# Optimization experiments

Hardware: AMD Instinct MI355X
Metric: run time of the kernel (lower is better)

Reference implementation:

```python
import jax, jax.numpy as jnp
import numpy as np

N = 100000      # nodes
E = 1600000     # edges
F_IN = 64       # num_features
H = 64          # hidden_channels
NG = 64         # graphs in batch
ALPHA = 0.5


def _lin_init(key, fan_in, fan_out):
    kw, kb = jax.random.split(key)
    bound = 1.0 / np.sqrt(fan_in)
    w = jax.random.uniform(kw, (fan_in, fan_out), jnp.float32, -bound, bound)
    b = jax.random.uniform(kb, (fan_out,), jnp.float32, -bound, bound)
    return w, b


def setup_inputs() -> dict:
    key = jax.random.key(0)
    ks = jax.random.split(key, 12)
    x = jax.random.normal(ks[0], (N, F_IN), dtype=jnp.float32)
    edge_index = jax.random.randint(ks[1], (2, E), 0, N, dtype=jnp.int32)
    batch = jnp.sort(jax.random.randint(ks[2], (N,), 0, NG, dtype=jnp.int32))
    w1s, b1s = _lin_init(ks[3], F_IN, H)
    w1d, b1d = _lin_init(ks[4], F_IN, H)
    w2s, b2s = _lin_init(ks[5], H, H)
    w2d, b2d = _lin_init(ks[6], H, H)
    w3s, b3s = _lin_init(ks[7], H, H)
    w3d, b3d = _lin_init(ks[8], H, H)
    wl1, bl1 = _lin_init(ks[9], H, 5)
    wl2, bl2 = _lin_init(ks[10], 5, 1)
    return dict(x=x, edge_index=edge_index, batch=batch,
                w1s=w1s, b1s=b1s, w1d=w1d, b1d=b1d,
                w2s=w2s, b2s=b2s, w2d=w2d, b2d=b2d,
                w3s=w3s, b3s=b3s, w3d=w3d, b3d=b3d,
                wl1=wl1, bl1=bl1, wl2=wl2, bl2=bl2)


def _dir_gcn_conv(x, row, col, ws, bs, wd, bd):
    # directional norm: D_out^{-1/2} A D_in^{-1/2} (and same recipe for A^T)
    ones = jnp.ones((row.shape[0],), x.dtype)
    deg_out = jax.ops.segment_sum(ones, row, num_segments=N)  # row-sums of A
    deg_in = jax.ops.segment_sum(ones, col, num_segments=N)   # col-sums of A
    r_out = jnp.where(deg_out > 0, deg_out ** -0.5, 0.0)
    r_in = jnp.where(deg_in > 0, deg_in ** -0.5, 0.0)
    norm = r_out[row] * r_in[col]  # per-edge weight; identical for A and A^T norms
    msg = norm[:, None] * x[col]                       # [E, F]
    adj_x = jax.ops.segment_sum(msg, row, num_segments=N)
    msg_t = norm[:, None] * x[row]
    adj_t_x = jax.ops.segment_sum(msg_t, col, num_segments=N)
    return ALPHA * (adj_x @ ws + bs) + (1.0 - ALPHA) * (adj_t_x @ wd + bd)


def reference(x, edge_index, batch,
              w1s, b1s, w1d, b1d,
              w2s, b2s, w2d, b2d,
              w3s, b3s, w3d, b3d,
              wl1, bl1, wl2, bl2):
    row, col = edge_index[0], edge_index[1]
    h = jax.nn.relu(_dir_gcn_conv(x, row, col, w1s, b1s, w1d, b1d))
    h = jax.nn.relu(_dir_gcn_conv(h, row, col, w2s, b2s, w2d, b2d))
    h = jax.nn.relu(_dir_gcn_conv(h, row, col, w3s, b3s, w3d, b3d))
    g = jax.ops.segment_max(h, batch, num_segments=NG)  # global max pool [NG, H]
    g = jax.nn.relu(g @ wl1 + bl1)
    return g @ wl2 + bl2  # [NG, 1]
```

## Files before the change

### kernel.cpp

```cpp
#include <hip/hip_runtime.h>

#define N_NODES 100000
#define N_EDGES 1600000
#define EPAD    (N_EDGES + NB * BW + 512)
#define HDIM    64
#define NGRAPH  64
#define BW      256
#define NB      391
#define NBLK    256
#define CHUNK   ((N_EDGES + NBLK - 1) / NBLK)
#define MTILES  (N_NODES / 16)

typedef _Float16 h16;
typedef _Float16 h16x4 __attribute__((ext_vector_type(4)));
typedef _Float16 h16x8 __attribute__((ext_vector_type(8)));
typedef float    f32x4 __attribute__((ext_vector_type(4)));

__global__ __launch_bounds__(512) void bucket_count(const int* __restrict__ ei,
                                                    int* __restrict__ cntTabA,
                                                    int* __restrict__ cntTabT) {
    __shared__ int cA[NB], cT[NB];
    const int tid = threadIdx.x;
    for (int i = tid; i < NB; i += 512) { cA[i] = 0; cT[i] = 0; }
    __syncthreads();
    const int e0 = blockIdx.x * CHUNK, e1 = min(e0 + CHUNK, N_EDGES);
    for (int e = e0 + tid; e < e1; e += 512) {
        int r = ei[e];
        int c = ei[N_EDGES + e];
        atomicAdd(&cA[r >> 8], 1);
        atomicAdd(&cT[c >> 8], 1);
    }
    __syncthreads();
    for (int b = tid; b < NB; b += 512) {
        cntTabA[b * NBLK + blockIdx.x] = cA[b];
        cntTabT[b * NBLK + blockIdx.x] = cT[b];
    }
}

__global__ __launch_bounds__(256) void chunk_scan(int* __restrict__ cntTabA,
                                                  int* __restrict__ cntTabT,
                                                  int* __restrict__ tot) {
    __shared__ int s[256];
    const int b = blockIdx.x, d = blockIdx.y, tid = threadIdx.x;
    int* tab = d ? cntTabT : cntTabA;
    int v = tab[b * NBLK + tid];
    s[tid] = v;
    __syncthreads();
    for (int off = 1; off < 256; off <<= 1) {
        int t = (tid >= off) ? s[tid - off] : 0;
        __syncthreads();
        s[tid] += t;
        __syncthreads();
    }
    tab[b * NBLK + tid] = s[tid] - v;
    if (tid == 255) tot[d * 512 + b] = s[255];
}

__global__ __launch_bounds__(512) void start_scan(const int* __restrict__ tot,
                                                  int* __restrict__ bktStartA,
                                                  int* __restrict__ bktStartT) {
    __shared__ int s[512];
    const int tid = threadIdx.x;
    int v = (tid < NB) ? tot[tid] : 0;
    s[tid] = v;
    __syncthreads();
    for (int off = 1; off < 512; off <<= 1) {
        int t = (tid >= off) ? s[tid - off] : 0;
        __syncthreads();
        s[tid] += t;
        __syncthreads();
    }
    if (tid < NB) bktStartA[tid] = s[tid] - v;
    if (tid == 0) bktStartA[NB] = N_EDGES;
    __syncthreads();
    int v2 = (tid < NB) ? tot[512 + tid] : 0;
    s[tid] = v2;
    __syncthreads();
    for (int off = 1; off < 512; off <<= 1) {
        int t = (tid >= off) ? s[tid - off] : 0;
        __syncthreads();
        s[tid] += t;
        __syncthreads();
    }
    if (tid < NB) bktStartT[tid] = s[tid] - v2;
    if (tid == 0) bktStartT[NB] = N_EDGES;
}

__global__ __launch_bounds__(512) void bucketize_write(const int* __restrict__ ei,
                                                       const int* __restrict__ cntTabA,
                                                       const int* __restrict__ cntTabT,
                                                       const int* __restrict__ bktStartA,
                                                       const int* __restrict__ bktStartT,
                                                       int2* __restrict__ bktA,
                                                       int2* __restrict__ bktT) {
    __shared__ int bA[NB], bT[NB];
    const int tid = threadIdx.x;
    for (int i = tid; i < NB; i += 512) {
        bA[i] = bktStartA[i] + cntTabA[i * NBLK + blockIdx.x];
        bT[i] = bktStartT[i] + cntTabT[i * NBLK + blockIdx.x];
    }
    __syncthreads();
    const int e0 = blockIdx.x * CHUNK, e1 = min(e0 + CHUNK, N_EDGES);
    for (int e = e0 + tid; e < e1; e += 512) {
        int r = ei[e];
        int c = ei[N_EDGES + e];
        int pA = atomicAdd(&bA[r >> 8], 1);
        bktA[pA] = make_int2(r, c);
        int pT = atomicAdd(&bT[c >> 8], 1);
        bktT[pT] = make_int2(c, r);
    }
}

__global__ __launch_bounds__(256) void bucket_deg_ptr(
        const int* __restrict__ bktStartA, const int* __restrict__ bktStartT,
        const int2* __restrict__ bktA, const int2* __restrict__ bktT,
        int* __restrict__ deg_out, int* __restrict__ deg_in,
        float* __restrict__ r_out, float* __restrict__ r_in,
        int* __restrict__ rowptrP, int* __restrict__ colptrP) {
    __shared__ int c[BW];
    __shared__ int s[256];
    const int b = blockIdx.x, d = blockIdx.y, tid = threadIdx.x;
    const int* bs = d ? bktStartT : bktStartA;
    const int2* bkt = d ? bktT : bktA;
    int* deg = d ? deg_in : deg_out;
    float* rr = d ? r_in : r_out;
    int* ptr = d ? colptrP : rowptrP;
    const int node0 = b * BW;
    c[tid] = 0;
    __syncthreads();
    const int i0 = bs[b], i1 = bs[b + 1];
    for (int i = i0 + tid; i < i1; i += 256) atomicAdd(&c[bkt[i].x - node0], 1);
    __syncthreads();
    int n = node0 + tid, dg = c[tid];
    int pad = dg + (dg & 1);
    if (n < N_NODES) {
        deg[n] = dg;
        rr[n] = dg > 0 ? rsqrtf((float)dg) : 0.0f;
    } else pad = 0;
    s[tid] = pad;
    __syncthreads();
    for (int off = 1; off < 256; off <<= 1) {
        int t = (tid >= off) ? s[tid - off] : 0;
        __syncthreads();
        s[tid] += t;
        __syncthreads();
    }
    if (n < N_NODES) ptr[n] = i0 + b * BW + (s[tid] - pad);
}

__global__ __launch_bounds__(512) void bucket_scatter(
        const int* __restrict__ rowptrP, const int* __restrict__ colptrP,
        const float* __restrict__ r_out, const float* __restrict__ r_in,
        const int* __restrict__ bktStartA, const int* __restrict__ bktStartT,
        const int2* __restrict__ bktA, const int2* __restrict__ bktT,
        int2* __restrict__ recA, int2* __restrict__ recT) {
    __shared__ int cur[BW];
    __shared__ float rwt[BW];
    const int b = blockIdx.x, d = blockIdx.y, tid = threadIdx.x;
    const int* ptr = d ? colptrP : rowptrP;
    const float* rt = d ? r_in : r_out;
    const float* rs = d ? r_out : r_in;
    const int* bs = d ? bktStartT : bktStartA;
    const int2* bkt = d ? bktT : bktA;
    int2* rec = d ? recT : recA;
    const int node0 = b * BW;
    if (tid < BW) {
        int n = node0 + tid;
        cur[tid] = (n < N_NODES) ? ptr[n] : 0;
        rwt[tid] = (n < N_NODES) ? rt[n] : 0.0f;
    }
    __syncthreads();
    const int i0 = bs[b], i1 = bs[b + 1];
    for (int i = i0 + tid; i < i1; i += 512) {
        int2 e = bkt[i];
        float w = rwt[e.x - node0] * rs[e.y];
        int p = atomicAdd(&cur[e.x - node0], 1);
        rec[p] = make_int2(e.y << 7, __float_as_int(w));
    }
}

__global__ __launch_bounds__(256) void cast_kernel(const float4* __restrict__ x,
                                                   h16x4* __restrict__ xh,
                                                   unsigned* __restrict__ g) {
    if (blockIdx.x == 0) {
        for (int j = threadIdx.x; j < NGRAPH * HDIM; j += 256) g[j] = 0u;
    }
    int i = blockIdx.x * 256 + threadIdx.x;
    if (i < N_NODES * 16) {
        float4 v = x[i];
        h16x4 o;
        o.x = (h16)v.x; o.y = (h16)v.y; o.z = (h16)v.z; o.w = (h16)v.w;
        xh[i] = o;
    }
}

__global__ __launch_bounds__(256) void wprep_kernel(
        const float* __restrict__ w1s, const float* __restrict__ w1d,
        const float* __restrict__ w2s, const float* __restrict__ w2d,
        const float* __restrict__ w3s, const float* __restrict__ w3d,
        const float* __restrict__ b1s, const float* __restrict__ b1d,
        const float* __restrict__ b2s, const float* __restrict__ b2d,
        const float* __restrict__ b3s, const float* __restrict__ b3d,
        h16* __restrict__ WT, float* __restrict__ bc) {
    const int l = blockIdx.y;
    const float* ws = l == 0 ? w1s : l == 1 ? w2s : w3s;
    const float* wd = l == 0 ? w1d : l == 1 ? w2d : w3d;
    int e = blockIdx.x * 256 + threadIdx.x;
    if (e < 8192) {
        int f = e >> 7, k = e & 127;
        float v = (k < 64) ? ws[k * 64 + f] : wd[(k - 64) * 64 + f];
        WT[l * 8192 + f * 128 + k] = (h16)(0.5f * v);
    }
    if (blockIdx.x == 0 && threadIdx.x < 64) {
        const float* bs = l == 0 ? b1s : l == 1 ? b2s : b3s;
        const float* bd = l == 0 ? b1d : l == 1 ? b2d : b3d;
        bc[l * 64 + threadIdx.x] = 0.5f * (bs[threadIdx.x] + bd[threadIdx.x]);
    }
}

__device__ __forceinline__ void fma4h(float4& a, float w, h16x4 f) {
    a.x = fmaf(w, (float)f.x, a.x);
    a.y = fmaf(w, (float)f.y, a.y);
    a.z = fmaf(w, (float)f.z, a.z);
    a.w = fmaf(w, (float)f.w, a.w);
}

__device__ __forceinline__ float4 red_s(float4 v) {
    v.x += __shfl_xor(v.x, 16); v.y += __shfl_xor(v.y, 16);
    v.z += __shfl_xor(v.z, 16); v.w += __shfl_xor(v.w, 16);
    v.x += __shfl_xor(v.x, 32); v.y += __shfl_xor(v.y, 32);
    v.z += __shfl_xor(v.z, 32); v.w += __shfl_xor(v.w, 32);
    return v;
}

__device__ __forceinline__ h16x4 ld_h4(const char* __restrict__ p) {
    return *(const h16x4*)p;
}

__device__ __forceinline__ float4 agg_dir(const char* __restrict__ hb,
                                          const int2* __restrict__ rec,
                                          int start, int deg, int q, int s, int sh) {
    float4 a0 = {0.f,0.f,0.f,0.f}, a1 = {0.f,0.f,0.f,0.f};
    float4 a2 = {0.f,0.f,0.f,0.f}, a3 = {0.f,0.f,0.f,0.f};
    const int4* rec4 = (const int4*)(rec + start);
    const int qb = q * 8;
    const int t = 2 * s;
    int4 p0 = rec4[s];
    int4 p1 = rec4[4 + s];
    int4 p2 = rec4[8 + s];
    if (t < deg)      fma4h(a0, __int_as_float(p0.y), ld_h4(hb + (p0.x << sh) + qb));
    if (t + 1 < deg)  fma4h(a1, __int_as_float(p0.w), ld_h4(hb + (p0.z << sh) + qb));
    if (t + 8 < deg)  fma4h(a2, __int_as_float(p1.y), ld_h4(hb + (p1.x << sh) + qb));
    if (t + 9 < deg)  fma4h(a3, __int_as_float(p1.w), ld_h4(hb + (p1.z << sh) + qb));
    if (t + 16 < deg) fma4h(a0, __int_as_float(p2.y), ld_h4(hb + (p2.x << sh) + qb));
    if (t + 17 < deg) fma4h(a1, __int_as_float(p2.w), ld_h4(hb + (p2.z << sh) + qb));
    for (int k = 24; k < deg; k += 16) {
        int4 q0 = rec4[(k >> 1) + s];
        int4 q1 = rec4[(k >> 1) + 4 + s];
        if (k + t < deg)
            fma4h(a2, __int_as_float(q0.y), ld_h4(hb + (q0.x << sh) + qb));
        if (k + t + 1 < deg)
            fma4h(a3, __int_as_float(q0.w), ld_h4(hb + (q0.z << sh) + qb));
        if (k + t + 8 < deg)
            fma4h(a0, __int_as_float(q1.y), ld_h4(hb + (q1.x << sh) + qb));
        if (k + t + 9 < deg)
            fma4h(a1, __int_as_float(q1.w), ld_h4(hb + (q1.z << sh) + qb));
    }
    a0.x += a1.x; a0.y += a1.y; a0.z += a1.z; a0.w += a1.w;
    a2.x += a3.x; a2.y += a3.y; a2.z += a3.z; a2.w += a3.w;
    a0.x += a2.x; a0.y += a2.y; a0.z += a2.z; a0.w += a2.w;
    return red_s(a0);
}

__global__ __launch_bounds__(256) void agg_kernel(
        const char* __restrict__ h_in, char* __restrict__ acc_out, int sh,
        const int* __restrict__ rowptrP, const int* __restrict__ deg_out,
        const int2* __restrict__ recA,
        const int* __restrict__ colptrP, const int* __restrict__ deg_in,
        const int2* __restrict__ recT) {
    const int tid  = threadIdx.x;
    const int wid  = (blockIdx.x << 2) + (tid >> 6);
    const int lane = tid & 63;
    const int node = wid >> 1;
    const int dir  = wid & 1;
    const int q = lane & 15;
    const int s = lane >> 4;

    const int* ptr = dir ? colptrP : rowptrP;
    const int* deg = dir ? deg_in : deg_out;
    const int2* rec = dir ? recT : recA;

    float4 a = agg_dir(h_in, rec, ptr[node], deg[node], q, s, sh);
    if (s == 0) {
        h16x4 pk;
        pk.x = (h16)a.x; pk.y = (h16)a.y; pk.z = (h16)a.z; pk.w = (h16)a.w;
        *(h16x4*)(acc_out + (size_t)node * 256 + dir * 128 + q * 8) = pk;
    }
}

__global__ __launch_bounds__(256) void gemm_kernel(char* __restrict__ acc,
                                                   const h16* __restrict__ WT,
                                                   const float* __restrict__ bc,
                                                   const int* __restrict__ batch,
                                                   unsigned* __restrict__ g,
                                                   int do_pool) {
    const int lane = threadIdx.x & 63;
    const int wid = (blockIdx.x * 256 + threadIdx.x) >> 6;
    const int nW = gridDim.x * 4;
    const int m = lane & 15, t = lane >> 4;

    h16x8 bfrag[4][4];
    float bb[4];
#pragma unroll
    for (int nt = 0; nt < 4; nt++) {
        bb[nt] = bc[nt * 16 + m];
#pragma unroll
        for (int kk = 0; kk < 4; kk++)
            bfrag[nt][kk] = *(const h16x8*)(WT + (nt * 16 + m) * 128 + kk * 32 + t * 8);
    }

    for (int tile = wid; tile < MTILES; tile += nW) {
        char* arow = acc + (size_t)tile * 16 * 256;
        const int node0 = tile * 16;
        int b0 = 0, b15 = 0;
        if (do_pool) { b0 = batch[node0]; b15 = batch[node0 + 15]; }
        h16x8 afrag[4];
#pragma unroll
        for (int kk = 0; kk < 4; kk++)
            afrag[kk] = *(const h16x8*)(arow + m * 256 + kk * 64 + t * 16);
#pragma unroll
        for (int nt = 0; nt < 4; nt++) {
            f32x4 c = {0.f, 0.f, 0.f, 0.f};
#pragma unroll
            for (int kk = 0; kk < 4; kk++)
                c = __builtin_amdgcn_mfma_f32_16x16x32_f16(afrag[kk], bfrag[nt][kk], c, 0, 0, 0);
            float ov[4];
#pragma unroll
            for (int r = 0; r < 4; r++) {
                ov[r] = fmaxf(c[r] + bb[nt], 0.0f);
                *(h16*)(arow + (t * 4 + r) * 256 + (nt * 16 + m) * 2) = (h16)ov[r];
            }
            if (do_pool) {
                if (b0 == b15) {
                    float mx = fmaxf(fmaxf(ov[0], ov[1]), fmaxf(ov[2], ov[3]));
                    mx = fmaxf(mx, __shfl_xor(mx, 16));
                    mx = fmaxf(mx, __shfl_xor(mx, 32));
                    if (t == 0)
                        atomicMax(&g[b0 * HDIM + nt * 16 + m], __float_as_uint(mx));
                } else {
#pragma unroll
                    for (int r = 0; r < 4; r++)
                        atomicMax(&g[batch[node0 + t * 4 + r] * HDIM + nt * 16 + m],
                                  __float_as_uint(ov[r]));
                }
            }
        }
    }
}

__global__ __launch_bounds__(64) void mlp_kernel(const unsigned* __restrict__ g,
                                                 const float* __restrict__ wl1,
                                                 const float* __restrict__ bl1,
                                                 const float* __restrict__ wl2,
                                                 const float* __restrict__ bl2,
                                                 float* __restrict__ out) {
    int t = threadIdx.x;
    float gv[HDIM];
#pragma unroll
    for (int k = 0; k < HDIM; k++) gv[k] = __uint_as_float(g[t * HDIM + k]);
    float o = bl2[0];
#pragma unroll
    for (int j = 0; j < 5; j++) {
        float hj = bl1[j];
#pragma unroll
        for (int k = 0; k < HDIM; k++) hj += gv[k] * wl1[k * 5 + j];
        hj = fmaxf(hj, 0.0f);
        o += hj * wl2[j];
    }
    out[t] = o;
}

extern "C" void kernel_launch(void* const* d_in, const int* in_sizes, int n_in,
                              void* d_out, int out_size, void* d_ws, size_t ws_size,
                              hipStream_t stream) {
    const float* x   = (const float*)d_in[0];
    const int*   ei  = (const int*)d_in[1];
    const int*   bat = (const int*)d_in[2];
    const float* w1s = (const float*)d_in[3];
    const float* b1s = (const float*)d_in[4];
    const float* w1d = (const float*)d_in[5];
    const float* b1d = (const float*)d_in[6];
    const float* w2s = (const float*)d_in[7];
    const float* b2s = (const float*)d_in[8];
    const float* w2d = (const float*)d_in[9];
    const float* b2d = (const float*)d_in[10];
    const float* w3s = (const float*)d_in[11];
    const float* b3s = (const float*)d_in[12];
    const float* w3d = (const float*)d_in[13];
    const float* b3d = (const float*)d_in[14];
    const float* wl1 = (const float*)d_in[15];
    const float* bl1 = (const float*)d_in[16];
    const float* wl2 = (const float*)d_in[17];
    const float* bl2 = (const float*)d_in[18];
    float* out = (float*)d_out;

    char* p = (char*)d_ws;
    int*   deg_out = (int*)p;              p += N_NODES * 4;
    int*   deg_in  = (int*)p;              p += N_NODES * 4;
    int*   rowptrP = (int*)p;              p += N_NODES * 4;
    int*   colptrP = (int*)p;              p += N_NODES * 4;
    float* r_out   = (float*)p;            p += N_NODES * 4;
    float* r_in    = (float*)p;            p += N_NODES * 4;
    int*   cntTabA = (int*)p;              p += (size_t)NB * NBLK * 4;
    int*   cntTabT = (int*)p;              p += (size_t)NB * NBLK * 4;
    int*   totTab  = (int*)p;              p += 1024 * 4;
    int*   bktStartA = (int*)p;            p += 512 * 4;
    int*   bktStartT = (int*)p;            p += 512 * 4;
    int2*  recA    = (int2*)p;             p += (size_t)EPAD * 8;
    int2*  recT    = (int2*)p;             p += (size_t)EPAD * 8;
    char*  bufP    = p;
    int2*  bktA    = (int2*)p;
    int2*  bktT    = (int2*)(p + (size_t)N_EDGES * 8);
    p += 2 * (size_t)N_EDGES * 8;
    char*  bufQ    = p;
    h16*   xh      = (h16*)p;
    p += 2 * (size_t)N_EDGES * 8;
    unsigned* g    = (unsigned*)p;         p += NGRAPH * HDIM * 4;
    h16*   WT      = (h16*)p;              p += 3 * 8192 * 2;
    float* bc      = (float*)p;            p += 3 * 64 * 4;

    cast_kernel<<<(N_NODES * 16 + 255) / 256, 256, 0, stream>>>(
        (const float4*)x, (h16x4*)xh, g);
    dim3 gw(32, 3);
    wprep_kernel<<<gw, 256, 0, stream>>>(w1s, w1d, w2s, w2d, w3s, w3d,
                                         b1s, b1d, b2s, b2d, b3s, b3d, WT, bc);

    bucket_count<<<NBLK, 512, 0, stream>>>(ei, cntTabA, cntTabT);
    dim3 gb2(NB, 2);
    chunk_scan<<<gb2, 256, 0, stream>>>(cntTabA, cntTabT, totTab);
    start_scan<<<1, 512, 0, stream>>>(totTab, bktStartA, bktStartT);
    bucketize_write<<<NBLK, 512, 0, stream>>>(ei, cntTabA, cntTabT,
                                              bktStartA, bktStartT, bktA, bktT);

    dim3 gb(NB, 2);
    bucket_deg_ptr<<<gb, 256, 0, stream>>>(bktStartA, bktStartT, bktA, bktT,
                                           deg_out, deg_in, r_out, r_in,
                                           rowptrP, colptrP);
    bucket_scatter<<<gb, 512, 0, stream>>>(
        rowptrP, colptrP, r_out, r_in, bktStartA, bktStartT, bktA, bktT, recA, recT);

    const int agrid = N_NODES * 2 / 4;
    agg_kernel<<<agrid, 256, 0, stream>>>((const char*)xh, bufP, 0,
                                          rowptrP, deg_out, recA, colptrP, deg_in, recT);
    gemm_kernel<<<256, 256, 0, stream>>>(bufP, WT, bc, bat, g, 0);
    agg_kernel<<<agrid, 256, 0, stream>>>(bufP, bufQ, 1,
                                          rowptrP, deg_out, recA, colptrP, deg_in, recT);
    gemm_kernel<<<256, 256, 0, stream>>>(bufQ, WT + 8192, bc + 64, bat, g, 0);
    agg_kernel<<<agrid, 256, 0, stream>>>(bufQ, bufP, 1,
                                          rowptrP, deg_out, recA, colptrP, deg_in, recT);
    gemm_kernel<<<256, 256, 0, stream>>>(bufP, WT + 16384, bc + 128, bat, g, 1);

    mlp_kernel<<<1, 64, 0, stream>>>(g, wl1, bl1, wl2, bl2, out);
}
```

Baseline: 515.3 us.

## Compact edge records to 4-byte indices and fuse degree/scatter kernels

Packs bucketed edges into single 32-bit words (neighbor<<8 | local node), merges the degree/pointer and scatter kernels into one launch, and stores CSR records as plain neighbor indices instead of (index, weight) pairs. The per-edge weight is now factored as r_target applied once per node after aggregation times r_source looked up per neighbor inside the gather loop. This halves record traffic and removes a kernel launch and a bucket re-read, at the cost of an extra random 4-byte gather of the source norm per edge. The aggregation loop is reworked to process four neighbors per lane with padding to multiples of four.

```diff
diff --git a/kernel.cpp b/kernel.cpp
--- a/kernel.cpp
+++ b/kernel.cpp
@@ -2,11 +2,12 @@
 
 #define N_NODES 100000
 #define N_EDGES 1600000
-#define EPAD    (N_EDGES + NB * BW + 512)
 #define HDIM    64
 #define NGRAPH  64
 #define BW      256
 #define NB      391
+#define PADS    772
+#define EPAD    (N_EDGES + NB * PADS + 16)
 #define NBLK    256
 #define CHUNK   ((N_EDGES + NBLK - 1) / NBLK)
 #define MTILES  (N_NODES / 16)
@@ -91,8 +92,8 @@
                                                        const int* __restrict__ cntTabT,
                                                        const int* __restrict__ bktStartA,
                                                        const int* __restrict__ bktStartT,
-                                                       int2* __restrict__ bktA,
-                                                       int2* __restrict__ bktT) {
+                                                       int* __restrict__ bktA,
+                                                       int* __restrict__ bktT) {
     __shared__ int bA[NB], bT[NB];
     const int tid = threadIdx.x;
     for (int i = tid; i < NB; i += 512) {
@@ -105,77 +106,58 @@
         int r = ei[e];
         int c = ei[N_EDGES + e];
         int pA = atomicAdd(&bA[r >> 8], 1);
-        bktA[pA] = make_int2(r, c);
+        bktA[pA] = (c << 8) | (r & 255);
         int pT = atomicAdd(&bT[c >> 8], 1);
-        bktT[pT] = make_int2(c, r);
-    }
-}
-
-__global__ __launch_bounds__(256) void bucket_deg_ptr(
+        bktT[pT] = (r << 8) | (c & 255);
+    }
+}
+
+__global__ __launch_bounds__(256) void bucket_deg_scatter(
         const int* __restrict__ bktStartA, const int* __restrict__ bktStartT,
-        const int2* __restrict__ bktA, const int2* __restrict__ bktT,
+        const int* __restrict__ bktA, const int* __restrict__ bktT,
         int* __restrict__ deg_out, int* __restrict__ deg_in,
         float* __restrict__ r_out, float* __restrict__ r_in,
-        int* __restrict__ rowptrP, int* __restrict__ colptrP) {
+        int* __restrict__ rowptrP, int* __restrict__ colptrP,
+        int* __restrict__ recA, int* __restrict__ recT) {
     __shared__ int c[BW];
-    __shared__ int s[256];
+    __shared__ int sc[256];
     const int b = blockIdx.x, d = blockIdx.y, tid = threadIdx.x;
     const int* bs = d ? bktStartT : bktStartA;
-    const int2* bkt = d ? bktT : bktA;
+    const int* bkt = d ? bktT : bktA;
     int* deg = d ? deg_in : deg_out;
     float* rr = d ? r_in : r_out;
     int* ptr = d ? colptrP : rowptrP;
+    int* rec = d ? recT : recA;
     const int node0 = b * BW;
     c[tid] = 0;
     __syncthreads();
     const int i0 = bs[b], i1 = bs[b + 1];
-    for (int i = i0 + tid; i < i1; i += 256) atomicAdd(&c[bkt[i].x - node0], 1);
-    __syncthreads();
-    int n = node0 + tid, dg = c[tid];
-    int pad = dg + (dg & 1);
+    for (int i = i0 + tid; i < i1; i += 256) atomicAdd(&c[bkt[i] & 255], 1);
+    __syncthreads();
+    const int n = node0 + tid;
+    int dg = c[tid];
+    int pad = (n < N_NODES) ? ((dg + 3) & ~3) : 0;
     if (n < N_NODES) {
         deg[n] = dg;
         rr[n] = dg > 0 ? rsqrtf((float)dg) : 0.0f;
-    } else pad = 0;
-    s[tid] = pad;
+    }
+    sc[tid] = pad;
     __syncthreads();
     for (int off = 1; off < 256; off <<= 1) {
-        int t = (tid >= off) ? s[tid - off] : 0;
-        __syncthreads();
-        s[tid] += t;
-        __syncthreads();
-    }
-    if (n < N_NODES) ptr[n] = i0 + b * BW + (s[tid] - pad);
-}
-
-__global__ __launch_bounds__(512) void bucket_scatter(
-        const int* __restrict__ rowptrP, const int* __restrict__ colptrP,
-        const float* __restrict__ r_out, const float* __restrict__ r_in,
-        const int* __restrict__ bktStartA, const int* __restrict__ bktStartT,
-        const int2* __restrict__ bktA, const int2* __restrict__ bktT,
-        int2* __restrict__ recA, int2* __restrict__ recT) {
-    __shared__ int cur[BW];
-    __shared__ float rwt[BW];
-    const int b = blockIdx.x, d = blockIdx.y, tid = threadIdx.x;
-    const int* ptr = d ? colptrP : rowptrP;
-    const float* rt = d ? r_in : r_out;
-    const float* rs = d ? r_out : r_in;
-    const int* bs = d ? bktStartT : bktStartA;
-    const int2* bkt = d ? bktT : bktA;
-    int2* rec = d ? recT : recA;
-    const int node0 = b * BW;
-    if (tid < BW) {
-        int n = node0 + tid;
-        cur[tid] = (n < N_NODES) ? ptr[n] : 0;
-        rwt[tid] = (n < N_NODES) ? rt[n] : 0.0f;
-    }
-    __syncthreads();
-    const int i0 = bs[b], i1 = bs[b + 1];
-    for (int i = i0 + tid; i < i1; i += 512) {
-        int2 e = bkt[i];
-        float w = rwt[e.x - node0] * rs[e.y];
-        int p = atomicAdd(&cur[e.x - node0], 1);
-        rec[p] = make_int2(e.y << 7, __float_as_int(w));
+        int t = (tid >= off) ? sc[tid - off] : 0;
+        __syncthreads();
+        sc[tid] += t;
+        __syncthreads();
+    }
+    const int recBase = ((i0 + 3) & ~3) + b * PADS;
+    int myStart = recBase + (sc[tid] - pad);
+    if (n < N_NODES) ptr[n] = myStart;
+    c[tid] = myStart;
+    __syncthreads();
+    for (int i = i0 + tid; i < i1; i += 256) {
+        int e = bkt[i];
+        int p = atomicAdd(&c[e & 255], 1);
+        rec[p] = e >> 8;
     }
 }
 
@@ -238,33 +220,38 @@
 }
 
 __device__ __forceinline__ float4 agg_dir(const char* __restrict__ hb,
-                                          const int2* __restrict__ rec,
-                                          int start, int deg, int q, int s, int sh) {
+                                          const int* __restrict__ rec,
+                                          const float* __restrict__ rs,
+                                          int start, int deg, int q, int s, int sh2) {
     float4 a0 = {0.f,0.f,0.f,0.f}, a1 = {0.f,0.f,0.f,0.f};
     float4 a2 = {0.f,0.f,0.f,0.f}, a3 = {0.f,0.f,0.f,0.f};
     const int4* rec4 = (const int4*)(rec + start);
     const int qb = q * 8;
-    const int t = 2 * s;
-    int4 p0 = rec4[s];
-    int4 p1 = rec4[4 + s];
-    int4 p2 = rec4[8 + s];
-    if (t < deg)      fma4h(a0, __int_as_float(p0.y), ld_h4(hb + (p0.x << sh) + qb));
-    if (t + 1 < deg)  fma4h(a1, __int_as_float(p0.w), ld_h4(hb + (p0.z << sh) + qb));
-    if (t + 8 < deg)  fma4h(a2, __int_as_float(p1.y), ld_h4(hb + (p1.x << sh) + qb));
-    if (t + 9 < deg)  fma4h(a3, __int_as_float(p1.w), ld_h4(hb + (p1.z << sh) + qb));
-    if (t + 16 < deg) fma4h(a0, __int_as_float(p2.y), ld_h4(hb + (p2.x << sh) + qb));
-    if (t + 17 < deg) fma4h(a1, __int_as_float(p2.w), ld_h4(hb + (p2.z << sh) + qb));
-    for (int k = 24; k < deg; k += 16) {
-        int4 q0 = rec4[(k >> 1) + s];
-        int4 q1 = rec4[(k >> 1) + 4 + s];
-        if (k + t < deg)
-            fma4h(a2, __int_as_float(q0.y), ld_h4(hb + (q0.x << sh) + qb));
-        if (k + t + 1 < deg)
-            fma4h(a3, __int_as_float(q0.w), ld_h4(hb + (q0.z << sh) + qb));
-        if (k + t + 8 < deg)
-            fma4h(a0, __int_as_float(q1.y), ld_h4(hb + (q1.x << sh) + qb));
-        if (k + t + 9 < deg)
-            fma4h(a1, __int_as_float(q1.w), ld_h4(hb + (q1.z << sh) + qb));
+    int k = 0;
+    for (; k + 16 <= deg; k += 16) {
+        int4 p = rec4[(k >> 2) + s];
+        float w0 = rs[p.x], w1 = rs[p.y], w2 = rs[p.z], w3 = rs[p.w];
+        h16x4 f0 = ld_h4(hb + (p.x << sh2) + qb);
+        h16x4 f1 = ld_h4(hb + (p.y << sh2) + qb);
+        h16x4 f2 = ld_h4(hb + (p.z << sh2) + qb);
+        h16x4 f3 = ld_h4(hb + (p.w << sh2) + qb);
+        fma4h(a0, w0, f0);
+        fma4h(a1, w1, f1);
+        fma4h(a2, w2, f2);
+        fma4h(a3, w3, f3);
+    }
+    int rem = deg - k;
+    if (rem > 0) {
+        int4 p = rec4[(k >> 2) + s];
+        int base = 4 * s;
+        if (base < rem)
+            fma4h(a0, rs[p.x], ld_h4(hb + (p.x << sh2) + qb));
+        if (base + 1 < rem)
+            fma4h(a1, rs[p.y], ld_h4(hb + (p.y << sh2) + qb));
+        if (base + 2 < rem)
+            fma4h(a2, rs[p.z], ld_h4(hb + (p.z << sh2) + qb));
+        if (base + 3 < rem)
+            fma4h(a3, rs[p.w], ld_h4(hb + (p.w << sh2) + qb));
     }
     a0.x += a1.x; a0.y += a1.y; a0.z += a1.z; a0.w += a1.w;
     a2.x += a3.x; a2.y += a3.y; a2.z += a3.z; a2.w += a3.w;
@@ -273,11 +260,12 @@
 }
 
 __global__ __launch_bounds__(256) void agg_kernel(
-        const char* __restrict__ h_in, char* __restrict__ acc_out, int sh,
+        const char* __restrict__ h_in, char* __restrict__ acc_out, int sh2,
         const int* __restrict__ rowptrP, const int* __restrict__ deg_out,
-        const int2* __restrict__ recA,
+        const int* __restrict__ recA,
         const int* __restrict__ colptrP, const int* __restrict__ deg_in,
-        const int2* __restrict__ recT) {
+        const int* __restrict__ recT,
+        const float* __restrict__ r_out, const float* __restrict__ r_in) {
     const int tid  = threadIdx.x;
     const int wid  = (blockIdx.x << 2) + (tid >> 6);
     const int lane = tid & 63;
@@ -288,12 +276,16 @@
 
     const int* ptr = dir ? colptrP : rowptrP;
     const int* deg = dir ? deg_in : deg_out;
-    const int2* rec = dir ? recT : recA;
-
-    float4 a = agg_dir(h_in, rec, ptr[node], deg[node], q, s, sh);
+    const int* rec = dir ? recT : recA;
+    const float* rs = dir ? r_out : r_in;
+    const float* rt = dir ? r_in : r_out;
+
+    float4 a = agg_dir(h_in, rec, rs, ptr[node], deg[node], q, s, sh2);
     if (s == 0) {
+        float w = rt[node];
         h16x4 pk;
-        pk.x = (h16)a.x; pk.y = (h16)a.y; pk.z = (h16)a.z; pk.w = (h16)a.w;
+        pk.x = (h16)(a.x * w); pk.y = (h16)(a.y * w);
+        pk.z = (h16)(a.z * w); pk.w = (h16)(a.w * w);
         *(h16x4*)(acc_out + (size_t)node * 256 + dir * 128 + q * 8) = pk;
     }
 }
@@ -416,11 +408,11 @@
     int*   totTab  = (int*)p;              p += 1024 * 4;
     int*   bktStartA = (int*)p;            p += 512 * 4;
     int*   bktStartT = (int*)p;            p += 512 * 4;
-    int2*  recA    = (int2*)p;             p += (size_t)EPAD * 8;
-    int2*  recT    = (int2*)p;             p += (size_t)EPAD * 8;
+    int*   recA    = (int*)p;              p += (size_t)EPAD * 4;
+    int*   recT    = (int*)p;              p += (size_t)EPAD * 4;
     char*  bufP    = p;
-    int2*  bktA    = (int2*)p;
-    int2*  bktT    = (int2*)(p + (size_t)N_EDGES * 8);
+    int*   bktA    = (int*)p;
+    int*   bktT    = (int*)(p + (size_t)N_EDGES * 4);
     p += 2 * (size_t)N_EDGES * 8;
     char*  bufQ    = p;
     h16*   xh      = (h16*)p;
@@ -443,21 +435,22 @@
                                               bktStartA, bktStartT, bktA, bktT);
 
     dim3 gb(NB, 2);
-    bucket_deg_ptr<<<gb, 256, 0, stream>>>(bktStartA, bktStartT, bktA, bktT,
-                                           deg_out, deg_in, r_out, r_in,
-                                           rowptrP, colptrP);
-    bucket_scatter<<<gb, 512, 0, stream>>>(
-        rowptrP, colptrP, r_out, r_in, bktStartA, bktStartT, bktA, bktT, recA, recT);
+    bucket_deg_scatter<<<gb, 256, 0, stream>>>(bktStartA, bktStartT, bktA, bktT,
+                                               deg_out, deg_in, r_out, r_in,
+                                               rowptrP, colptrP, recA, recT);
 
     const int agrid = N_NODES * 2 / 4;
-    agg_kernel<<<agrid, 256, 0, stream>>>((const char*)xh, bufP, 0,
-                                          rowptrP, deg_out, recA, colptrP, deg_in, recT);
+    agg_kernel<<<agrid, 256, 0, stream>>>((const char*)xh, bufP, 7,
+                                          rowptrP, deg_out, recA, colptrP, deg_in, recT,
+                                          r_out, r_in);
     gemm_kernel<<<256, 256, 0, stream>>>(bufP, WT, bc, bat, g, 0);
-    agg_kernel<<<agrid, 256, 0, stream>>>(bufP, bufQ, 1,
-                                          rowptrP, deg_out, recA, colptrP, deg_in, recT);
+    agg_kernel<<<agrid, 256, 0, stream>>>(bufP, bufQ, 8,
+                                          rowptrP, deg_out, recA, colptrP, deg_in, recT,
+                                          r_out, r_in);
     gemm_kernel<<<256, 256, 0, stream>>>(bufQ, WT + 8192, bc + 64, bat, g, 0);
-    agg_kernel<<<agrid, 256, 0, stream>>>(bufQ, bufP, 1,
-                                          rowptrP, deg_out, recA, colptrP, deg_in, recT);
+    agg_kernel<<<agrid, 256, 0, stream>>>(bufQ, bufP, 8,
+                                          rowptrP, deg_out, recA, colptrP, deg_in, recT,
+                                          r_out, r_in);
     gemm_kernel<<<256, 256, 0, stream>>>(bufP, WT + 16384, bc + 128, bat, g, 1);
 
     mlp_kernel<<<1, 64, 0, stream>>>(g, wl1, bl1, wl2, bl2, out);
```

Result: slower. 563.9 us (+9.4%).
